# Optimization experiments

Hardware: AMD Instinct MI355X
Metric: run time of the kernel (lower is better)

## Reference

```python
import jax, jax.numpy as jnp
import numpy as np

P = 7          # corr_size (patch size)
PAD = P // 2   # displacement radius
PP = P * P     # 49 correlation channels
CHANS = [512, 1024, 512, 256, 256, 256]
HW = [64, 32, 16, 8, 4, 2]
B = 8


def _spatial_correlation(f1, f2):
    """out[b, pi*P+pj, y, x] = sum_c f1[b,c,y,x] * f2[b,c,y+pi-PAD, x+pj-PAD] (zero pad)."""
    Bb, C, H, W = f1.shape
    f2p = jnp.pad(f2, ((0, 0), (0, 0), (PAD, PAD), (PAD, PAD)))
    outs = [jnp.sum(f1 * f2p[:, :, di:di + H, dj:dj + W], axis=1)
            for di in range(P) for dj in range(P)]
    return jnp.stack(outs, axis=1)  # [B, P*P, H, W]


def _corr_lstm_cell(feat, feat_pre, h_pre, c_pre, w, b):
    corr = jax.nn.leaky_relu(_spatial_correlation(feat, feat_pre), 0.01)  # [B,49,H,W]
    lstm_in = jnp.concatenate([corr, h_pre], axis=1)                      # [B,98,H,W]
    conv = jax.lax.conv_general_dilated(
        lstm_in, w, window_strides=(1, 1), padding='SAME',
        dimension_numbers=('NCHW', 'OIHW', 'NCHW')) + b[None, :, None, None]
    cc_i, cc_f, cc_o, cc_g = jnp.split(conv, 4, axis=1)
    i = jax.nn.sigmoid(cc_i)
    f = jax.nn.sigmoid(cc_f)
    o = jax.nn.sigmoid(cc_o)
    g = jnp.tanh(cc_g)
    c_next = f * c_pre + i * g
    h_next = o * jnp.tanh(c_next)
    return h_next, c_next, corr


def setup_inputs() -> dict:
    key = jax.random.key(0)
    ks = jax.random.split(key, 6 * 6)
    d = {}
    ki = 0
    for l in range(6):
        C, S = CHANS[l], HW[l]
        d[f'x{l}'] = 0.05 * jax.random.normal(ks[ki], (B, C, S, S), jnp.float32); ki += 1
        d[f'xp{l}'] = 0.05 * jax.random.normal(ks[ki], (B, C, S, S), jnp.float32); ki += 1
        d[f'h{l}'] = 0.1 * jax.random.normal(ks[ki], (B, PP, S, S), jnp.float32); ki += 1
        d[f'c{l}'] = 0.1 * jax.random.normal(ks[ki], (B, PP, S, S), jnp.float32); ki += 1
        fan_in = 2 * PP * 9
        lim = float(np.sqrt(6.0 / (fan_in + 4 * PP * 9)))
        d[f'w{l}'] = jax.random.uniform(ks[ki], (4 * PP, 2 * PP, 3, 3), jnp.float32, -lim, lim); ki += 1
        bias = jnp.zeros((4 * PP,), jnp.float32).at[PP:2 * PP].set(1.0)  # forget-gate bias = 1
        d[f'b{l}'] = bias; ki += 1
    return d


def reference(x0, x1, x2, x3, x4, x5,
              xp0, xp1, xp2, xp3, xp4, xp5,
              h0, h1, h2, h3, h4, h5,
              c0, c1, c2, c3, c4, c5,
              w0, w1, w2, w3, w4, w5,
              b0, b1, b2, b3, b4, b5):
    xs = [x0, x1, x2, x3, x4, x5]
    xps = [xp0, xp1, xp2, xp3, xp4, xp5]
    hs = [h0, h1, h2, h3, h4, h5]
    cs = [c0, c1, c2, c3, c4, c5]
    ws = [w0, w1, w2, w3, w4, w5]
    bs = [b0, b1, b2, b3, b4, b5]
    outs = []
    for l in range(6):
        outs.append(_corr_lstm_cell(xs[l], xps[l], hs[l], cs[l], ws[l], bs[l]))
    h_next = tuple(o[0] for o in outs)
    c_next = tuple(o[1] for o in outs)
    corrs = tuple(o[2] for o in outs)
    return h_next + c_next + corrs  # flat 18-tuple
```

## Files before the change

kernel.cpp:

```cpp
#include <hip/hip_runtime.h>
#include <stdint.h>

#define DEV __device__ __forceinline__

typedef _Float16 half2_t __attribute__((ext_vector_type(2)));
typedef _Float16 half4_t __attribute__((ext_vector_type(4)));
typedef __bf16   bf16x8  __attribute__((ext_vector_type(8)));
typedef float    floatx4 __attribute__((ext_vector_type(4)));
typedef float    floatx2 __attribute__((ext_vector_type(2)));

DEV float fdot2f(half2_t a, half2_t b, float c) {
#if __has_builtin(__builtin_amdgcn_fdot2)
  return __builtin_amdgcn_fdot2(a, b, c, false);
#else
  return c + (float)a[0] * (float)b[0] + (float)a[1] * (float)b[1];
#endif
}

DEV half2_t pkh2(float a, float b) {
#if __has_builtin(__builtin_amdgcn_cvt_pkrtz)
  return __builtin_bit_cast(half2_t, __builtin_amdgcn_cvt_pkrtz(a, b));
#else
  half2_t r; r[0] = (_Float16)a; r[1] = (_Float16)b; return r;
#endif
}

DEV uint32_t f2bf(float f) {
  uint32_t u = __float_as_uint(f);
  return (u + 0x7FFFu + ((u >> 16) & 1u)) >> 16;
}

DEV void tile_barrier() {
  __builtin_amdgcn_sched_barrier(0);
  asm volatile("s_waitcnt lgkmcnt(0)" ::: "memory");
  __builtin_amdgcn_s_barrier();
  __builtin_amdgcn_sched_barrier(0);
}

struct CorrCfg {
  const float* gx[6]; const float* gxp[6];
  int wg_start[2];
  int mid_start;
  int small_start[3];
  int S[2], C[2], tiles_x[2], tiles_pb[2], cpl[2];
  int mcpl;
  int sS[3], sC[3], sNspl[3];
  long long poff[2], mpoff, spoff[3];
  const float* w[6];
  uint16_t* wpk;
  uint16_t* lstmz;
  int aux_start, nmemset_blk;
};

__global__ __launch_bounds__(256)
void corr_kernel(CorrCfg cfg, _Float16* __restrict__ partial)
{
  __shared__ half2_t ldsbuf[2][2][22*40] __attribute__((aligned(16)));
  const int tid = threadIdx.x;
  int wg = blockIdx.x;

  if (wg >= cfg.aux_start) {
    int aw = wg - cfg.aux_start;
    if (aw < cfg.nmemset_blk) {
      floatx4* p = (floatx4*)cfg.lstmz;
      p[(size_t)aw*256 + tid] = (floatx4)0.f;
    } else {
      int idx = (aw - cfg.nmemset_blk)*256 + tid;
      int lvl = idx / 258048;
      int e = idx - lvl*258048;
      const float* W = cfg.w[lvl];
      int j = e & 7, lane = (e >> 3) & 63, rest = e >> 9;
      int s = rest % 36, tt = rest / 36;
      int n  = tt*16 + (lane & 15);
      int ch = (s & 3)*32 + (lane >> 4)*8 + j;
      int tap = s >> 2, ky = tap/3, kx = tap - 3*ky;
      float v = 0.f;
      if (n < 196 && ch < 98) v = W[((n*98 + ch)*3 + ky)*3 + kx];
      cfg.wpk[idx] = (uint16_t)f2bf(v);
    }
    return;
  }

  if (wg >= cfg.small_start[0]) {
    int lvl = (wg >= cfg.small_start[2]) ? 2 : (wg >= cfg.small_start[1]) ? 1 : 0;
    long long i = (long long)(wg - cfg.small_start[lvl])*256 + tid;
    const int S = cfg.sS[lvl], C = cfg.sC[lvl], SS = S*S;
    const int nsp = cfg.sNspl[lvl];
    const long long per = (long long)8*49*SS;
    if (i >= (long long)nsp*per) return;
    int sp = (int)(i / per);
    long long rem = i - (long long)sp*per;
    const int cpl = C / nsp, cbase = sp * cpl;
    const float* X  = cfg.gx[lvl+3];
    const float* XP = cfg.gxp[lvl+3];
    int xc_ = (int)(rem % S); int yc = (int)((rem/S) % S);
    int d = (int)((rem/SS) % 49); int b = (int)(rem/((long long)49*SS));
    int yy = yc + d/7 - 3, xx = xc_ + (d%7) - 3;
    float s = 0.f;
    if (yy >= 0 && yy < S && xx >= 0 && xx < S) {
      const float* xb = X  + ((size_t)b*C + cbase)*SS + (size_t)yc*S + xc_;
      const float* pb = XP + ((size_t)b*C + cbase)*SS + (size_t)yy*S + xx;
      #pragma unroll 8
      for (int c = 0; c < cpl; ++c) s += xb[(size_t)c*SS] * pb[(size_t)c*SS];
    }
    partial[cfg.spoff[lvl] + (long long)sp*per + rem] = (_Float16)s;
    return;
  }

  if (wg >= cfg.mid_start) {
    constexpr int NT = 256, MS = 16, MC = 512;
    constexpr int ROWS = 22, COLS = 22, ST = 23;
    constexpr int SLOTS = ROWS * 6 * 2;
    constexpr int PER = 2;
    int rel = wg - cfg.mid_start;
    const int cpl = cfg.mcpl;
    const int sp = rel >> 3;
    const int b = rel & 7;
    const int tx = tid & 15, ty = tid >> 4;
    const int cbase = sp * cpl;
    const size_t SS = (size_t)MS*MS;
    const float* Xb  = cfg.gx[2]  + (size_t)b*MC*SS;
    const float* XPb = cfg.gxp[2] + (size_t)b*MC*SS;
    const size_t qoff = (size_t)ty*MS + tx;

    int f_go[PER], f_base[PER], f_col0[PER], f_pr[PER];
    bool f_ok[PER], f_val[PER];
    #pragma unroll
    for (int s = 0; s < PER; ++s) {
      int i = tid + s*NT;
      bool val = (i < SLOTS);
      int ii = val ? i : 0;
      int pr = ii & 1;
      int rest = ii >> 1;
      int q = rest % 6;
      int r = rest / 6;
      int gy = r - 3;
      int gx0 = -4 + 4*q;
      bool ok = val && gy >= 0 && gy < MS && gx0 >= 0 && (gx0 + 3) < MS;
      f_val[s] = val; f_ok[s] = ok; f_pr[s] = pr;
      f_go[s] = ok ? gy*MS + gx0 : 0;
      f_col0[s] = 4*q - 1;
      f_base[s] = r*ST;
    }

    float acc[49];
    #pragma unroll
    for (int d = 0; d < 49; ++d) acc[d] = 0.f;
    half2_t pk[PER][4];
    half2_t xq0[2], xq1[2];

#define MFILL_LOADPK(c0v) { \
  _Pragma("unroll") for (int s = 0; s < PER; ++s) { \
    const float* p_ = XPb + (size_t)(cbase + (c0v) + 2*f_pr[s])*SS + f_go[s]; \
    floatx4 a_ = (floatx4)0.f, b2_ = (floatx4)0.f; \
    if (f_ok[s]) { a_ = *(const floatx4*)p_; b2_ = *(const floatx4*)(p_ + SS); } \
    _Pragma("unroll") for (int j = 0; j < 4; ++j) \
      pk[s][j] = pkh2(a_[j], b2_[j]); } }

#define MXLOADPK(dst, c0v) { \
  float t0_ = Xb[(size_t)(cbase + (c0v) + 0)*SS + qoff]; \
  float t1_ = Xb[(size_t)(cbase + (c0v) + 1)*SS + qoff]; \
  float t2_ = Xb[(size_t)(cbase + (c0v) + 2)*SS + qoff]; \
  float t3_ = Xb[(size_t)(cbase + (c0v) + 3)*SS + qoff]; \
  dst[0] = pkh2(t0_, t1_); dst[1] = pkh2(t2_, t3_); }

#define MFILL_STORE(bbv) { \
  _Pragma("unroll") for (int s = 0; s < PER; ++s) if (f_val[s]) { \
    half2_t* plane_ = &ldsbuf[bbv][f_pr[s]][0]; \
    _Pragma("unroll") for (int j = 0; j < 4; ++j) { \
      int col_ = f_col0[s] + j; \
      if (col_ >= 0 && col_ < COLS) \
        plane_[f_base[s] + col_] = pk[s][j]; } } }

#define MCOMPUTE(bbv, xq) { \
  _Pragma("unroll") for (int pr = 0; pr < 2; ++pr) { \
    half2_t xv = xq[pr]; \
    _Pragma("unroll") for (int di = 0; di < 7; ++di) { \
      const half2_t* row_ = &ldsbuf[bbv][pr][(ty+di)*ST + tx]; \
      _Pragma("unroll") for (int dj = 0; dj < 7; ++dj) \
        acc[di*7+dj] = fdot2f(xv, row_[dj], acc[di*7+dj]); } } }

    const int nchunk = cpl >> 2;
    MFILL_LOADPK(0); MXLOADPK(xq0, 0);
    MFILL_STORE(0);
    MFILL_LOADPK(4); MXLOADPK(xq1, 4);
    tile_barrier();
    for (int k = 0; k < nchunk; k += 2) {
      {
        if (k+1 < nchunk) MFILL_STORE(1);
        if (k+2 < nchunk) MFILL_LOADPK((k+2)*4);
        MCOMPUTE(0, xq0);
        if (k+2 < nchunk) MXLOADPK(xq0, (k+2)*4);
        tile_barrier();
      }
      if (k+1 < nchunk) {
        if (k+2 < nchunk) MFILL_STORE(0);
        if (k+3 < nchunk) MFILL_LOADPK((k+3)*4);
        MCOMPUTE(1, xq1);
        if (k+3 < nchunk) MXLOADPK(xq1, (k+3)*4);
        tile_barrier();
      }
    }
#undef MFILL_LOADPK
#undef MXLOADPK
#undef MFILL_STORE
#undef MCOMPUTE

    _Float16* P = partial + cfg.mpoff + ((size_t)sp*8 + b)*49*SS + qoff;
    #pragma unroll
    for (int d = 0; d < 49; ++d) P[(size_t)d*SS] = (_Float16)acc[d];
    return;
  }

  {
    constexpr int NT = 256, TH = 16, TW = 32;
    constexpr int ROWS = TH + 6;
    constexpr int COLS = TW + 6;
    constexpr int QUADS = 10;
    constexpr int ST = TW + 8;
    constexpr int SLOTS = ROWS * QUADS * 2;
    constexpr int PER = 2;

    int lvl = (wg >= cfg.wg_start[1]) ? 1 : 0;
    wg -= cfg.wg_start[lvl];
    const float* X  = cfg.gx[lvl];
    const float* XP = cfg.gxp[lvl];
    const int S = cfg.S[lvl], C = cfg.C[lvl];
    const int txc = cfg.tiles_x[lvl], tpb = cfg.tiles_pb[lvl], cpl = cfg.cpl[lvl];
    const int per_split = 8 * tpb;
    const int sp = wg / per_split;
    const int rem = wg - sp*per_split;
    const int b = rem / tpb;
    const int t = rem - b*tpb;
    const int y0 = (t / txc) * TH, x0t = (t % txc) * TW;
    const int tx = tid & 15, ty = tid >> 4;
    const int cbase = sp * cpl;
    const size_t SS = (size_t)S*S;
    const float* Xb  = X  + (size_t)b*C*SS;
    const float* XPb = XP + (size_t)b*C*SS;
    const int py = y0 + ty, px = x0t + 2*tx;
    const size_t qoff = (size_t)py*S + px;

    int f_go[PER], f_base[PER], f_col0[PER], f_pr[PER];
    bool f_ok[PER], f_val[PER];
    #pragma unroll
    for (int s = 0; s < PER; ++s) {
      int i = tid + s*NT;
      bool val = (i < SLOTS);
      int ii = val ? i : 0;
      int pr = ii & 1;
      int rest = ii >> 1;
      int q = rest % QUADS;
      int r = rest / QUADS;
      int gy = y0 + r - 3;
      int gx0 = x0t - 4 + 4*q;
      bool ok = val && gy >= 0 && gy < S && gx0 >= 0 && (gx0 + 3) < S;
      f_val[s] = val; f_ok[s] = ok; f_pr[s] = pr;
      f_go[s] = ok ? gy*S + gx0 : 0;
      f_col0[s] = 4*q - 1;
      f_base[s] = r*ST;
    }

    floatx2 acc[49];
    #pragma unroll
    for (int d = 0; d < 49; ++d) acc[d] = (floatx2)0.f;
    half2_t pk[PER][4];
    half2_t xq0[4], xq1[4];

#define FILL_LOADPK(c0v) { \
  _Pragma("unroll") for (int s = 0; s < PER; ++s) { \
    const float* p_ = XPb + (size_t)(cbase + (c0v) + 2*f_pr[s])*SS + f_go[s]; \
    floatx4 a_ = (floatx4)0.f, b2_ = (floatx4)0.f; \
    if (f_ok[s]) { a_ = *(const floatx4*)p_; b2_ = *(const floatx4*)(p_ + SS); } \
    _Pragma("unroll") for (int j = 0; j < 4; ++j) \
      pk[s][j] = pkh2(a_[j], b2_[j]); } }

#define XLOADPK(dst, c0v) { \
  floatx2 t0_ = *(const floatx2*)(Xb + (size_t)(cbase + (c0v) + 0)*SS + qoff); \
  floatx2 t1_ = *(const floatx2*)(Xb + (size_t)(cbase + (c0v) + 1)*SS + qoff); \
  floatx2 t2_ = *(const floatx2*)(Xb + (size_t)(cbase + (c0v) + 2)*SS + qoff); \
  floatx2 t3_ = *(const floatx2*)(Xb + (size_t)(cbase + (c0v) + 3)*SS + qoff); \
  dst[0] = pkh2(t0_.x, t1_.x); dst[1] = pkh2(t0_.y, t1_.y); \
  dst[2] = pkh2(t2_.x, t3_.x); dst[3] = pkh2(t2_.y, t3_.y); }

#define FILL_STORE(bbv) { \
  _Pragma("unroll") for (int s = 0; s < PER; ++s) if (f_val[s]) { \
    half2_t* plane_ = &ldsbuf[bbv][f_pr[s]][0]; \
    _Pragma("unroll") for (int j = 0; j < 4; ++j) { \
      int col_ = f_col0[s] + j; \
      if (col_ >= 0 && col_ < COLS) \
        plane_[f_base[s] + col_] = pk[s][j]; } } }

#define COMPUTE(bbv, xq) { \
  _Pragma("unroll") for (int pr = 0; pr < 2; ++pr) { \
    half2_t xqa = xq[2*pr], xqb = xq[2*pr+1]; \
    _Pragma("unroll") for (int di = 0; di < 7; ++di) { \
      const half2_t* row_ = &ldsbuf[bbv][pr][(ty+di)*ST + 2*tx]; \
      half2_t L_[8]; \
      _Pragma("unroll") for (int k = 0; k < 4; ++k) { \
        half4_t v_ = *(const half4_t*)(row_ + 2*k); \
        L_[2*k]   = __builtin_shufflevector(v_, v_, 0, 1); \
        L_[2*k+1] = __builtin_shufflevector(v_, v_, 2, 3); } \
      _Pragma("unroll") for (int dj = 0; dj < 7; ++dj) { \
        acc[di*7+dj].x = fdot2f(xqa, L_[dj],   acc[di*7+dj].x); \
        acc[di*7+dj].y = fdot2f(xqb, L_[dj+1], acc[di*7+dj].y); } } } }

    const int nchunk = cpl >> 2;
    FILL_LOADPK(0); XLOADPK(xq0, 0);
    FILL_STORE(0);
    FILL_LOADPK(4); XLOADPK(xq1, 4);
    tile_barrier();
    for (int k = 0; k < nchunk; k += 2) {
      {
        if (k+1 < nchunk) FILL_STORE(1);
        if (k+2 < nchunk) FILL_LOADPK((k+2)*4);
        COMPUTE(0, xq0);
        if (k+2 < nchunk) XLOADPK(xq0, (k+2)*4);
        tile_barrier();
      }
      if (k+1 < nchunk) {
        if (k+2 < nchunk) FILL_STORE(0);
        if (k+3 < nchunk) FILL_LOADPK((k+3)*4);
        COMPUTE(1, xq1);
        if (k+3 < nchunk) XLOADPK(xq1, (k+3)*4);
        tile_barrier();
      }
    }
#undef FILL_LOADPK
#undef XLOADPK
#undef FILL_STORE
#undef COMPUTE

    _Float16* P = partial + cfg.poff[lvl] + ((size_t)sp*8 + b)*49*SS + qoff;
    #pragma unroll
    for (int d = 0; d < 49; ++d) {
      half2_t pko = pkh2(acc[d].x, acc[d].y);
      *(uint32_t*)(P + (size_t)d*SS) = *(const uint32_t*)&pko;
    }
  }
}

struct P2Cfg {
  int blk_start[7];
  int S[6], nsplit[6], pxg[6], lg[6], gpb[6];
  long long poff[6], lstm_off[6], corr_off[6];
  const float* h[6];
};
__global__ __launch_bounds__(256)
void pass2_kernel(P2Cfg cfg, const _Float16* __restrict__ partial,
                  uint32_t* __restrict__ lstm, float* __restrict__ dout)
{
  __shared__ float lds[64*99];
  int blk = blockIdx.x;
  int lvl = 0;
  while (lvl < 5 && blk >= cfg.blk_start[lvl+1]) ++lvl;
  int rel = blk - cfg.blk_start[lvl];
  const int S = cfg.S[lvl], Sp = S + 2, SS = S*S;
  const int PXG = cfg.pxg[lvl], lg = cfg.lg[lvl], gpb = cfg.gpb[lvl];
  const int b = rel / gpb, g = rel - b*gpb;
  const int pixbase = g * PXG;
  const int tid = threadIdx.x;
  const int nsp = cfg.nsplit[lvl];
  const size_t spstride = (size_t)8*49*SS;
  const int quads = PXG >> 2;
  const int lq = lg - 2;
  for (int e = tid; e < quads*98; e += 256) {
    int qx = e & (quads - 1);
    int ch = e >> lq;
    int pix = pixbase + 4*qx;
    floatx4 v;
    if (ch < 49) {
      const _Float16* P = partial + cfg.poff[lvl] + ((size_t)b*49 + ch)*SS + pix;
      floatx4 s = (floatx4)0.f;
      for (int sp = 0; sp < nsp; ++sp) {
        half4_t pv = *(const half4_t*)(P + (size_t)sp*spstride);
        s[0] += (float)pv[0]; s[1] += (float)pv[1];
        s[2] += (float)pv[2]; s[3] += (float)pv[3];
      }
      #pragma unroll
      for (int j = 0; j < 4; ++j) s[j] = s[j] < 0.f ? 0.01f*s[j] : s[j];
      *(floatx4*)(dout + cfg.corr_off[lvl] + ((size_t)b*49 + ch)*SS + pix) = s;
      v = s;
    } else {
      v = *(const floatx4*)(cfg.h[lvl] + ((size_t)b*49 + (ch - 49))*SS + pix);
    }
    int pxl = 4*qx;
    lds[(pxl+0)*99 + ch] = v[0];
    lds[(pxl+1)*99 + ch] = v[1];
    lds[(pxl+2)*99 + ch] = v[2];
    lds[(pxl+3)*99 + ch] = v[3];
  }
  __syncthreads();
  uint32_t* Lb = lstm + (cfg.lstm_off[lvl] >> 1);
  for (int f = tid; f < (PXG << 6); f += 256) {
    int pxl = f >> 6, c2 = f & 63;
    int pix = pixbase + pxl;
    int y = pix / S, x = pix - y*S;
    int c0 = 2*c2, c1 = c0 + 1;
    float v0 = c0 < 98 ? lds[pxl*99 + c0] : 0.f;
    float v1 = c1 < 98 ? lds[pxl*99 + c1] : 0.f;
    Lb[((size_t)(b*Sp + y + 1)*Sp + (x + 1))*64 + c2] = f2bf(v0) | (f2bf(v1) << 16);
  }
}

struct CCfg {
  int wg_start[7];
  int S[6], tiles_x[6], tiles_pb[6], lwsh[6], mfc[6], mgrp[6];
  long long lstm_off[6], wp_off[6], h_off[6], c_off[6];
  const float* cpre[6]; const float* bias[6];
};
__global__ __launch_bounds__(256)
void conv_kernel(CCfg cfg, const uint16_t* __restrict__ lstm,
                 const uint16_t* __restrict__ wpack, float* __restrict__ dout)
{
  __shared__ float gl[224*69];
  int wg = blockIdx.x;
  int lvl = 0;
  while (lvl < 5 && wg >= cfg.wg_start[lvl+1]) ++lvl;
  wg -= cfg.wg_start[lvl];
  const int S = cfg.S[lvl], Sp = S + 2;
  const int lwsh = cfg.lwsh[lvl], msk = (1 << lwsh) - 1;
  const int tpb = cfg.tiles_pb[lvl];
  const int b = wg / tpb, t = wg - b*tpb;
  const int ty0 = (t / cfg.tiles_x[lvl]) << (6 - lwsh);
  const int tx0 = (t % cfg.tiles_x[lvl]) << lwsh;
  const int tid = threadIdx.x;
  const int wave = tid >> 6, lane = tid & 63;
  const int nhalf = wave & 1, mhalf = wave >> 1;
  const int mfc = cfg.mfc[lvl];
  const bool active = (mhalf < cfg.mgrp[lvl]);
  const int mi = lane & 15, q = lane >> 4;
  const int SS = S*S;
  const int ntc = 7 - nhalf;

  if (active) {
    const uint16_t* lb = lstm + cfg.lstm_off[lvl] + (size_t)b*Sp*Sp*128;
    int aoff[2];
    #pragma unroll
    for (int mf = 0; mf < 2; ++mf) {
      int p = mhalf*32 + mf*16 + mi;
      int pc = p < SS ? p : 0;
      int y = ty0 + (pc >> lwsh), xx = tx0 + (pc & msk);
      aoff[mf] = (y*Sp + xx)*128 + q*8;
    }
    const uint16_t* wb = wpack + cfg.wp_off[lvl]
                       + (size_t)(nhalf*7)*36*512 + (size_t)lane*8;
    floatx4 acc[2][7];
    #pragma unroll
    for (int mf = 0; mf < 2; ++mf)
      #pragma unroll
      for (int nt = 0; nt < 7; ++nt) acc[mf][nt] = (floatx4)0.0f;

#define CONV_LOAD(sv, AV, BV) { \
  int tap_ = (sv) >> 2, cs_ = (sv) & 3; \
  int ky_ = tap_ / 3, kx_ = tap_ - 3*ky_; \
  int ao_ = ((ky_*Sp + kx_) << 7) + (cs_ << 5); \
  _Pragma("unroll") for (int mf = 0; mf < 2; ++mf) \
    if (mf < mfc) AV[mf] = *(const bf16x8*)(lb + aoff[mf] + ao_); \
  _Pragma("unroll") for (int nt = 0; nt < 7; ++nt) \
    if (nt < ntc) BV[nt] = *(const bf16x8*)(wb + (size_t)((nt)*36 + (sv))*512); }

#define CONV_MFMA(AV, BV) { \
  _Pragma("unroll") for (int nt = 0; nt < 7; ++nt) \
    _Pragma("unroll") for (int mf = 0; mf < 2; ++mf) \
      if (nt < ntc && mf < mfc) acc[mf][nt] = __builtin_amdgcn_mfma_f32_16x16x32_bf16( \
                        AV[mf], BV[nt], acc[mf][nt], 0, 0, 0); }

    bf16x8 av0[2], bv0[7], av1[2], bv1[7];
    CONV_LOAD(0, av0, bv0);
    for (int s = 0; s < 36; s += 2) {
      CONV_LOAD(s+1, av1, bv1);
      CONV_MFMA(av0, bv0);
      if (s+2 < 36) CONV_LOAD(s+2, av0, bv0);
      CONV_MFMA(av1, bv1);
    }
#undef CONV_LOAD
#undef CONV_MFMA

    #pragma unroll
    for (int mf = 0; mf < 2; ++mf) {
      if (mf < mfc) {
        #pragma unroll
        for (int nt = 0; nt < 7; ++nt) {
          const int n = nhalf*112 + nt*16 + mi;
          if (n < 196) {
            #pragma unroll
            for (int r = 0; r < 4; ++r) {
              const int p = mhalf*32 + mf*16 + q*4 + r;
              gl[n*69 + p] = acc[mf][nt][r];
            }
          }
        }
      }
    }
  }
  __syncthreads();

  const int p2 = lane;
  const int grp = wave;
  if (p2 < SS) {
    const int y = ty0 + (p2 >> lwsh), xx = tx0 + (p2 & msk);
    const int pix = y*S + xx;
    const float* bb2 = cfg.bias[lvl];
    const float* cp  = cfg.cpre[lvl];
    const int ch0 = grp*13, chend = (grp == 3) ? 49 : grp*13 + 13;
    for (int ch = ch0; ch < chend; ++ch) {
      float ci  = gl[ch*69 + p2]        + bb2[ch];
      float cf  = gl[(ch+49)*69 + p2]   + bb2[ch+49];
      float co_ = gl[(ch+98)*69 + p2]   + bb2[ch+98];
      float cg  = gl[(ch+147)*69 + p2]  + bb2[ch+147];
      float ig = 1.f/(1.f + __expf(-ci));
      float fg = 1.f/(1.f + __expf(-cf));
      float og = 1.f/(1.f + __expf(-co_));
      float g  = 1.f - 2.f/(__expf(2.f*cg) + 1.f);
      size_t e = ((size_t)b*49 + ch)*SS + pix;
      float cpv = cp[e];
      float cn = fg*cpv + ig*g;
      float hn = og * (1.f - 2.f/(__expf(2.f*cn) + 1.f));
      dout[cfg.h_off[lvl] + e] = hn;
      dout[cfg.c_off[lvl] + e] = cn;
    }
  }
}

extern "C" void kernel_launch(void* const* d_in, const int* in_sizes, int n_in,
                              void* d_out, int out_size, void* d_ws, size_t ws_size,
                              hipStream_t stream)
{
  const float *x[6], *xp[6], *h[6], *cpre[6], *w[6], *bias[6];
  for (int l = 0; l < 6; ++l) {
    x[l]    = (const float*)d_in[6*l + 0];
    xp[l]   = (const float*)d_in[6*l + 1];
    h[l]    = (const float*)d_in[6*l + 2];
    cpre[l] = (const float*)d_in[6*l + 3];
    w[l]    = (const float*)d_in[6*l + 4];
    bias[l] = (const float*)d_in[6*l + 5];
  }
  static const int SL[6] = {64,32,16,8,4,2};
  static const int CL[6] = {512,1024,512,256,256,256};
  int NSPL[6] = {8,16,16,1,1,1};

  long long hsz[6], lstm_off[6], h_off[6], poff[6];
  long long a1 = 0, a3 = 0;
  for (int l = 0; l < 6; ++l) {
    int S = SL[l], Sp = S + 2;
    hsz[l] = 8LL*49*S*S;
    lstm_off[l] = a1; a1 += 8LL*Sp*Sp*128;
    h_off[l]    = a3; a3 += hsz[l];
  }
  long long pa = 0;
  for (int l = 0; l < 6; ++l) { poff[l] = pa; pa += (long long)NSPL[l]*hsz[l]; }
  {
    long long need = a1*2 + 6LL*258048*2 + pa*2;
    if (need > (long long)ws_size) {
      NSPL[0] = 4; NSPL[1] = 8; NSPL[2] = 16;
      pa = 0;
      for (int l = 0; l < 6; ++l) { poff[l] = pa; pa += (long long)NSPL[l]*hsz[l]; }
    }
  }
  const long long GRP = a3;
  const long long LSTM_ELEMS = a1;

  uint16_t* lstm  = (uint16_t*)d_ws;
  uint16_t* wpack = (uint16_t*)((char*)d_ws + LSTM_ELEMS*2);
  _Float16* partial = (_Float16*)((char*)d_ws + LSTM_ELEMS*2 + 6LL*258048*2);
  float* dout = (float*)d_out;

  {
    CorrCfg ccfg;
    static const int tpb2[2] = {8, 2};
    static const int txx2[2] = {2, 1};
    for (int l = 0; l < 6; ++l) { ccfg.gx[l] = x[l]; ccfg.gxp[l] = xp[l]; }
    int start = 0;
    for (int l = 0; l < 2; ++l) {
      ccfg.wg_start[l] = start;
      ccfg.S[l] = SL[l]; ccfg.C[l] = CL[l];
      ccfg.tiles_x[l] = txx2[l]; ccfg.tiles_pb[l] = tpb2[l];
      ccfg.cpl[l] = CL[l]/NSPL[l];
      ccfg.poff[l] = poff[l];
      start += NSPL[l]*8*tpb2[l];
    }
    ccfg.mid_start = start;
    ccfg.mcpl = CL[2]/NSPL[2];
    ccfg.mpoff = poff[2];
    start += NSPL[2]*8;
    for (int l = 0; l < 3; ++l) {
      ccfg.small_start[l] = start;
      ccfg.sS[l] = SL[l+3]; ccfg.sC[l] = CL[l+3];
      ccfg.sNspl[l] = NSPL[l+3];
      ccfg.spoff[l] = poff[l+3];
      start += (int)((NSPL[l+3]*hsz[l+3] + 255)/256);
    }
    for (int l = 0; l < 6; ++l) ccfg.w[l] = w[l];
    ccfg.wpk = wpack;
    ccfg.lstmz = lstm;
    ccfg.aux_start = start;
    ccfg.nmemset_blk = (int)(LSTM_ELEMS / 8 / 256);
    int npack_blk = 6048;
    int grid = start + ccfg.nmemset_blk + npack_blk;
    corr_kernel<<<grid, 256, 0, stream>>>(ccfg, partial);
  }
  {
    P2Cfg p2; int start = 0;
    static const int PXGL[6] = {32,64,64,64,16,4};
    static const int LGL[6]  = {5,6,6,6,4,2};
    for (int l = 0; l < 6; ++l) {
      p2.blk_start[l] = start;
      int gpb = (SL[l]*SL[l]) / PXGL[l]; if (gpb < 1) gpb = 1;
      p2.gpb[l] = gpb;
      start += 8 * gpb;
      p2.S[l] = SL[l]; p2.nsplit[l] = NSPL[l];
      p2.pxg[l] = PXGL[l]; p2.lg[l] = LGL[l];
      p2.poff[l] = poff[l]; p2.lstm_off[l] = lstm_off[l];
      p2.corr_off[l] = 2*GRP + h_off[l];
      p2.h[l] = h[l];
    }
    p2.blk_start[6] = start;
    pass2_kernel<<<start, 256, 0, stream>>>(p2, partial, (uint32_t*)lstm, dout);
  }
  {
    CCfg cc;
    static const int ctpb[6] = {64, 16, 4, 1, 1, 1};
    static const int ctx[6]  = {4, 2, 1, 1, 1, 1};
    static const int clw[6]  = {4, 4, 4, 3, 2, 1};
    static const int cmfc[6] = {2, 2, 2, 2, 1, 1};
    static const int cmg[6]  = {2, 2, 2, 2, 1, 1};
    int start = 0;
    for (int l = 0; l < 6; ++l) {
      cc.wg_start[l] = start; start += 8*ctpb[l];
      cc.S[l] = SL[l]; cc.tiles_x[l] = ctx[l]; cc.tiles_pb[l] = ctpb[l];
      cc.lwsh[l] = clw[l]; cc.mfc[l] = cmfc[l]; cc.mgrp[l] = cmg[l];
      cc.lstm_off[l] = lstm_off[l];
      cc.wp_off[l] = 258048LL*l;
      cc.h_off[l] = h_off[l];
      cc.c_off[l] = GRP + h_off[l];
      cc.cpre[l] = cpre[l];
      cc.bias[l] = bias[l];
    }
    cc.wg_start[6] = start;
    conv_kernel<<<start, 256, 0, stream>>>(cc, lstm, wpack, dout);
  }
  (void)in_sizes; (void)n_in; (void)out_size; (void)ws_size;
}
```

Before: 430.8 us.

## Split conv N-tiles across 8 waves with 512-thread blocks

```diff
diff --git a/kernel.cpp b/kernel.cpp
--- a/kernel.cpp
+++ b/kernel.cpp
@@ -409,11 +409,11 @@
   long long lstm_off[6], wp_off[6], h_off[6], c_off[6];
   const float* cpre[6]; const float* bias[6];
 };
-__global__ __launch_bounds__(256)
+__global__ __launch_bounds__(512)
 void conv_kernel(CCfg cfg, const uint16_t* __restrict__ lstm,
                  const uint16_t* __restrict__ wpack, float* __restrict__ dout)
 {
-  __shared__ float gl[224*69];
+  __shared__ float gl[196*69];
   int wg = blockIdx.x;
   int lvl = 0;
   while (lvl < 5 && wg >= cfg.wg_start[lvl+1]) ++lvl;
@@ -425,13 +425,14 @@
   const int ty0 = (t / cfg.tiles_x[lvl]) << (6 - lwsh);
   const int tx0 = (t % cfg.tiles_x[lvl]) << lwsh;
   const int tid = threadIdx.x;
-  const int wave = tid >> 6, lane = tid & 63;
-  const int nhalf = wave & 1, mhalf = wave >> 1;
+  const int wv = tid >> 6, lane = tid & 63;
+  const int mhalf = wv >> 2, nhalf = (wv >> 1) & 1, ntg = wv & 1;
   const int mfc = cfg.mfc[lvl];
   const bool active = (mhalf < cfg.mgrp[lvl]);
   const int mi = lane & 15, q = lane >> 4;
   const int SS = S*S;
-  const int ntc = 7 - nhalf;
+  const int ntb = ntg * 4;
+  const int ntn = (ntg == 0) ? 4 : (3 - nhalf);
 
   if (active) {
     const uint16_t* lb = lstm + cfg.lstm_off[lvl] + (size_t)b*Sp*Sp*128;
@@ -444,12 +445,12 @@
       aoff[mf] = (y*Sp + xx)*128 + q*8;
     }
     const uint16_t* wb = wpack + cfg.wp_off[lvl]
-                       + (size_t)(nhalf*7)*36*512 + (size_t)lane*8;
-    floatx4 acc[2][7];
+                       + (size_t)(nhalf*7 + ntb)*36*512 + (size_t)lane*8;
+    floatx4 acc[2][4];
     #pragma unroll
     for (int mf = 0; mf < 2; ++mf)
       #pragma unroll
-      for (int nt = 0; nt < 7; ++nt) acc[mf][nt] = (floatx4)0.0f;
+      for (int j = 0; j < 4; ++j) acc[mf][j] = (floatx4)0.0f;
 
 #define CONV_LOAD(sv, AV, BV) { \
   int tap_ = (sv) >> 2, cs_ = (sv) & 3; \
@@ -457,16 +458,16 @@
   int ao_ = ((ky_*Sp + kx_) << 7) + (cs_ << 5); \
   _Pragma("unroll") for (int mf = 0; mf < 2; ++mf) \
     if (mf < mfc) AV[mf] = *(const bf16x8*)(lb + aoff[mf] + ao_); \
-  _Pragma("unroll") for (int nt = 0; nt < 7; ++nt) \
-    if (nt < ntc) BV[nt] = *(const bf16x8*)(wb + (size_t)((nt)*36 + (sv))*512); }
+  _Pragma("unroll") for (int j = 0; j < 4; ++j) \
+    if (j < ntn) BV[j] = *(const bf16x8*)(wb + (size_t)((j)*36 + (sv))*512); }
 
 #define CONV_MFMA(AV, BV) { \
-  _Pragma("unroll") for (int nt = 0; nt < 7; ++nt) \
+  _Pragma("unroll") for (int j = 0; j < 4; ++j) \
     _Pragma("unroll") for (int mf = 0; mf < 2; ++mf) \
-      if (nt < ntc && mf < mfc) acc[mf][nt] = __builtin_amdgcn_mfma_f32_16x16x32_bf16( \
-                        AV[mf], BV[nt], acc[mf][nt], 0, 0, 0); }
-
-    bf16x8 av0[2], bv0[7], av1[2], bv1[7];
+      if (j < ntn && mf < mfc) acc[mf][j] = __builtin_amdgcn_mfma_f32_16x16x32_bf16( \
+                        AV[mf], BV[j], acc[mf][j], 0, 0, 0); }
+
+    bf16x8 av0[2], bv0[4], av1[2], bv1[4];
     CONV_LOAD(0, av0, bv0);
     for (int s = 0; s < 36; s += 2) {
       CONV_LOAD(s+1, av1, bv1);
@@ -481,13 +482,15 @@
     for (int mf = 0; mf < 2; ++mf) {
       if (mf < mfc) {
         #pragma unroll
-        for (int nt = 0; nt < 7; ++nt) {
-          const int n = nhalf*112 + nt*16 + mi;
-          if (n < 196) {
-            #pragma unroll
-            for (int r = 0; r < 4; ++r) {
-              const int p = mhalf*32 + mf*16 + q*4 + r;
-              gl[n*69 + p] = acc[mf][nt][r];
+        for (int j = 0; j < 4; ++j) {
+          if (j < ntn) {
+            const int n = nhalf*112 + (ntb + j)*16 + mi;
+            if (n < 196) {
+              #pragma unroll
+              for (int r = 0; r < 4; ++r) {
+                const int p = mhalf*32 + mf*16 + q*4 + r;
+                gl[n*69 + p] = acc[mf][j][r];
+              }
             }
           }
         }
@@ -497,13 +500,12 @@
   __syncthreads();
 
   const int p2 = lane;
-  const int grp = wave;
   if (p2 < SS) {
     const int y = ty0 + (p2 >> lwsh), xx = tx0 + (p2 & msk);
     const int pix = y*S + xx;
     const float* bb2 = cfg.bias[lvl];
     const float* cp  = cfg.cpre[lvl];
-    const int ch0 = grp*13, chend = (grp == 3) ? 49 : grp*13 + 13;
+    const int ch0 = (wv*49) >> 3, chend = ((wv+1)*49) >> 3;
     for (int ch = ch0; ch < chend; ++ch) {
       float ci  = gl[ch*69 + p2]        + bb2[ch];
       float cf  = gl[(ch+49)*69 + p2]   + bb2[ch+49];
@@ -638,7 +640,7 @@
       cc.bias[l] = bias[l];
     }
     cc.wg_start[6] = start;
-    conv_kernel<<<start, 256, 0, stream>>>(cc, lstm, wpack, dout);
+    conv_kernel<<<start, 512, 0, stream>>>(cc, lstm, wpack, dout);
   }
   (void)in_sizes; (void)n_in; (void)out_size; (void)ws_size;
 }
```

Measured after the change: 431.6 us. Within noise of the previous version (+0.2%).
